# Kernel tuning notes

Measured on AMD Instinct MI355X. Metric: run time of the kernel, lower is better.

## Reference

```python
import jax, jax.numpy as jnp
import numpy as np

N1 = 50000
N2 = 50000
NN = 16
NI = 64
ND = 128


def setup_inputs() -> dict:
    key = jax.random.key(0)
    ks = jax.random.split(key, 12)
    inp = {
        "features1": jax.random.normal(ks[0], (N1, NI), dtype=jnp.float32),
        "features2": jax.random.normal(ks[1], (N2, NI), dtype=jnp.float32),
        "x1": jax.random.normal(ks[2], (N1, 3), dtype=jnp.float32),
        "x2": jax.random.normal(ks[3], (N2, 3), dtype=jnp.float32),
        "nuv1": jax.random.normal(ks[4], (N1, 3, 3), dtype=jnp.float32),
        "nuv2": jax.random.normal(ks[5], (N2, 3, 3), dtype=jnp.float32),
        "topk": jax.random.randint(ks[6], (N1, NN), 0, N2, dtype=jnp.int64),
        # query_f params: Linear(2*Ni, Nd) -> ELU -> Linear(Nd, Nd) -> ELU
        "W1": jax.random.normal(ks[7], (2 * NI, ND), dtype=jnp.float32) * (1.0 / np.sqrt(2 * NI)),
        "b1": jnp.zeros((ND,), dtype=jnp.float32),
        "W2": jax.random.normal(ks[8], (ND, ND), dtype=jnp.float32) * (1.0 / np.sqrt(ND)),
        "b2": jnp.zeros((ND,), dtype=jnp.float32),
        "radius": jnp.float32(1.0),
    }
    return inp


def reference(features1, features2, x1, x2, nuv1, nuv2, topk, W1, b1, W2, b2, radius):
    # gather neighbor features: [N1, nn, Ni]
    feats_nn = features2[topk]
    # concat with self features broadcast over neighbor axis: [N1, nn, 2*Ni]
    feat_self = jnp.broadcast_to(features1[:, None, :], feats_nn.shape)
    h = jnp.concatenate([feats_nn, feat_self], axis=-1)
    # small fused MLP (query_f)
    h = jax.nn.elu(h @ W1 + b1)
    h = jax.nn.elu(h @ W2 + b2)  # [N1, nn, Nd]
    # distance-weighted aggregation
    x_nn = x2[topk]                          # [N1, nn, 3]
    orient = x_nn - x1[:, None, :]
    dis2 = jnp.sum(orient * orient, axis=2)  # [N1, nn]
    w = jnp.exp(-dis2 / (2.0 * radius * radius))
    w = jnp.where(topk == 0, jnp.float32(0.0), w)  # mask padded (index-0) neighbors
    # weighted matmul reduction: [N1, Nd]
    out = jnp.einsum("nk,nkd->nd", w, h)
    return out
```

## Files before the change

kernel.cpp:

```cpp
#include <hip/hip_runtime.h>

#define N1C 50000
#define N2C 50000
#define NNC 16
#define NIC 64
#define NDC 128
#define QB  8
#define MR  128
#define FELEMS (N1C * NIC)

typedef __bf16 bf16x8 __attribute__((ext_vector_type(8)));
typedef float f32x4 __attribute__((ext_vector_type(4)));
typedef unsigned u32x4 __attribute__((ext_vector_type(4)));

#if defined(__has_builtin)
#if __has_builtin(__builtin_amdgcn_cvt_pk_bf16_f32)
#define HAVE_PK_BF16 1
#endif
#endif

#ifdef HAVE_PK_BF16
typedef __bf16 bf16x2 __attribute__((ext_vector_type(2)));
static __device__ __forceinline__ unsigned int pkbf(float a, float b) {
    bf16x2 r = __builtin_amdgcn_cvt_pk_bf16_f32(a, b);
    return __builtin_bit_cast(unsigned int, r);
}
#else
static __device__ __forceinline__ unsigned short f2bf_sw(float f) {
    unsigned int u = __builtin_bit_cast(unsigned int, f);
    u += 0x7fffu + ((u >> 16) & 1u);
    return (unsigned short)(u >> 16);
}
static __device__ __forceinline__ unsigned int pkbf(float a, float b) {
    return (unsigned int)f2bf_sw(a) | ((unsigned int)f2bf_sw(b) << 16);
}
#endif

static __device__ __forceinline__ float elu(float x) {
    return x > 0.f ? x : __expf(x) - 1.f;
}

__global__ void prep_w(const float* __restrict__ W1, const float* __restrict__ W2,
                       unsigned short* __restrict__ wsW) {
    const int idx = blockIdx.x * 256 + threadIdx.x;
    const int m   = idx >> 14;
    const int o   = idx & 16383;
    const int d   = o >> 7;
    const int k   = o & 127;
    const float* W = m ? W2 : W1;
    wsW[idx] = (unsigned short)pkbf(W[(size_t)k * NDC + d], 0.f);
}

__global__ void prep_f(const float* __restrict__ f1, const float* __restrict__ f2,
                       unsigned short* __restrict__ dst) {
    const int g = blockIdx.x * 256 + threadIdx.x;
    const size_t base = (size_t)g * 8;
    const float* src = (base < FELEMS) ? (f1 + base) : (f2 + base - FELEMS);
    const float4 v0 = *(const float4*)src;
    const float4 v1 = *(const float4*)(src + 4);
    uint4 o;
    o.x = pkbf(v0.x, v0.y);
    o.y = pkbf(v0.z, v0.w);
    o.z = pkbf(v1.x, v1.y);
    o.w = pkbf(v1.z, v1.w);
    *(uint4*)(dst + base) = o;
}

static __device__ __forceinline__ int swz(int o) {
    return (o & ~15) | ((o + (o >> 4)) & 15);
}

__global__ __launch_bounds__(256, 4)
void fused_knn_mlp(const unsigned short* __restrict__ f1b,
                   const unsigned short* __restrict__ f2b,
                   const float* __restrict__ x1,
                   const float* __restrict__ x2,
                   const int*   __restrict__ topk,
                   const float* __restrict__ b1,
                   const float* __restrict__ b2,
                   const float* __restrict__ radius,
                   const unsigned short* __restrict__ wsW,
                   float* __restrict__ out)
{
    __shared__ uint4 sW[2048];

    const int tid  = threadIdx.x;
    const int blk  = blockIdx.x;
    const int lane = tid & 63;
    const int wave = tid >> 6;
    const int quad = lane >> 4;
    const int l16  = lane & 15;
    const int rloc = wave * 32 + l16;

    const int idx0 = topk[blk * MR + rloc];
    const int idx1 = topk[blk * MR + rloc + 16];
    const int q0   = blk * QB + wave * 2;
    const int q1   = q0 + 1;

    uint4 xf0[4], xf1[4];
    #pragma unroll
    for (int ks = 0; ks < 2; ++ks) {
        xf0[ks] = *(const uint4*)(f2b + (size_t)idx0 * NIC + ks * 32 + quad * 8);
        xf1[ks] = *(const uint4*)(f2b + (size_t)idx1 * NIC + ks * 32 + quad * 8);
        xf0[ks + 2] = *(const uint4*)(f1b + (size_t)q0 * NIC + ks * 32 + quad * 8);
        xf1[ks + 2] = *(const uint4*)(f1b + (size_t)q1 * NIC + ks * 32 + quad * 8);
    }

    {
        const uint4* wp = (const uint4*)wsW;
        #pragma unroll
        for (int it = 0; it < 8; ++it) {
            const int o = it * 256 + tid;
            sW[swz(o)] = wp[o];
        }
    }

    float wg0, wg1;
    {
        const float rr = radius[0];
        const float inv2r2 = 1.f / (2.f * rr * rr);
        const float dx0 = x2[idx0 * 3 + 0] - x1[q0 * 3 + 0];
        const float dy0 = x2[idx0 * 3 + 1] - x1[q0 * 3 + 1];
        const float dz0 = x2[idx0 * 3 + 2] - x1[q0 * 3 + 2];
        const float dx1 = x2[idx1 * 3 + 0] - x1[q1 * 3 + 0];
        const float dy1 = x2[idx1 * 3 + 1] - x1[q1 * 3 + 1];
        const float dz1 = x2[idx1 * 3 + 2] - x1[q1 * 3 + 2];
        wg0 = (idx0 == 0) ? 0.f : __expf(-(dx0 * dx0 + dy0 * dy0 + dz0 * dz0) * inv2r2);
        wg1 = (idx1 == 0) ? 0.f : __expf(-(dx1 * dx1 + dy1 * dy1 + dz1 * dz1) * inv2r2);
    }

    __syncthreads();

    f32x4 acc[8][2];
    #pragma unroll
    for (int mt = 0; mt < 8; ++mt) {
        acc[mt][0] = (f32x4){0.f, 0.f, 0.f, 0.f};
        acc[mt][1] = acc[mt][0];
    }
    #pragma unroll
    for (int ks = 0; ks < 4; ++ks) {
        const bf16x8 x0 = __builtin_bit_cast(bf16x8, xf0[ks]);
        const bf16x8 x1v = __builtin_bit_cast(bf16x8, xf1[ks]);
        #pragma unroll
        for (int mt = 0; mt < 8; ++mt) {
            const bf16x8 a = *(const bf16x8*)&sW[(mt * 16 + l16) * 16 + ((ks * 4 + quad + l16) & 15)];
            acc[mt][0] = __builtin_amdgcn_mfma_f32_16x16x32_bf16(a, x0, acc[mt][0], 0, 0, 0);
            acc[mt][1] = __builtin_amdgcn_mfma_f32_16x16x32_bf16(a, x1v, acc[mt][1], 0, 0, 0);
        }
    }

    __syncthreads();

    uint4 w2t[8];
    {
        const uint4* wp2 = ((const uint4*)wsW) + 2048;
        #pragma unroll
        for (int it = 0; it < 8; ++it)
            w2t[it] = wp2[it * 256 + tid];
    }

    unsigned P[8][2][2];
    #pragma unroll
    for (int mt = 0; mt < 8; ++mt) {
        const float4 b1v = *(const float4*)(b1 + mt * 16 + quad * 4);
        #pragma unroll
        for (int nt = 0; nt < 2; ++nt) {
            P[mt][nt][0] = pkbf(elu(acc[mt][nt][0] + b1v.x), elu(acc[mt][nt][1] + b1v.y));
            P[mt][nt][1] = pkbf(elu(acc[mt][nt][2] + b1v.z), elu(acc[mt][nt][3] + b1v.w));
        }
    }

    #pragma unroll
    for (int it = 0; it < 8; ++it)
        sW[swz(it * 256 + tid)] = w2t[it];
    __syncthreads();

    f32x4 acc2[2][8];
    #pragma unroll
    for (int nt2 = 0; nt2 < 8; ++nt2) {
        acc2[0][nt2] = (f32x4){0.f, 0.f, 0.f, 0.f};
        acc2[1][nt2] = acc2[0][nt2];
    }
    #pragma unroll
    for (int ks = 0; ks < 4; ++ks) {
        u32x4 a2[2];
        #pragma unroll
        for (int mt2 = 0; mt2 < 2; ++mt2) {
            #pragma unroll
            for (int u = 0; u < 4; ++u) {
                const int src = (((quad * 2) + (u >> 1)) & 3) * 16 + l16;
                const unsigned lo = __shfl(P[2 * ks][mt2][u & 1], src, 64);
                const unsigned hi = __shfl(P[2 * ks + 1][mt2][u & 1], src, 64);
                a2[mt2][u] = (quad & 2) ? hi : lo;
            }
        }
        const bf16x8 af0 = __builtin_bit_cast(bf16x8, a2[0]);
        const bf16x8 af1 = __builtin_bit_cast(bf16x8, a2[1]);
        #pragma unroll
        for (int nt2 = 0; nt2 < 8; ++nt2) {
            const bf16x8 b = *(const bf16x8*)&sW[(nt2 * 16 + l16) * 16 + ((ks * 4 + quad + l16) & 15)];
            acc2[0][nt2] = __builtin_amdgcn_mfma_f32_16x16x32_bf16(af0, b, acc2[0][nt2], 0, 0, 0);
            acc2[1][nt2] = __builtin_amdgcn_mfma_f32_16x16x32_bf16(af1, b, acc2[1][nt2], 0, 0, 0);
        }
    }

    float wk0[4], wk1[4];
    #pragma unroll
    for (int reg = 0; reg < 4; ++reg) {
        const int src = (lane & 48) | (quad * 4 + reg);
        wk0[reg] = __shfl(wg0, src, 64);
        wk1[reg] = __shfl(wg1, src, 64);
    }
    #pragma unroll
    for (int mt2 = 0; mt2 < 2; ++mt2) {
        #pragma unroll
        for (int nt2 = 0; nt2 < 8; ++nt2) {
            const int d2 = nt2 * 16 + l16;
            const float bb = b2[d2];
            float s;
            if (mt2 == 0)
                s = elu(acc2[0][nt2][0] + bb) * wk0[0] + elu(acc2[0][nt2][1] + bb) * wk0[1]
                  + elu(acc2[0][nt2][2] + bb) * wk0[2] + elu(acc2[0][nt2][3] + bb) * wk0[3];
            else
                s = elu(acc2[1][nt2][0] + bb) * wk1[0] + elu(acc2[1][nt2][1] + bb) * wk1[1]
                  + elu(acc2[1][nt2][2] + bb) * wk1[2] + elu(acc2[1][nt2][3] + bb) * wk1[3];
            s += __shfl_xor(s, 16, 64);
            s += __shfl_xor(s, 32, 64);
            if (lane < 16) {
                out[(size_t)(blk * QB + wave * 2 + mt2) * NDC + d2] = s;
            }
        }
    }
}

extern "C" void kernel_launch(void* const* d_in, const int* in_sizes, int n_in,
                              void* d_out, int out_size, void* d_ws, size_t ws_size,
                              hipStream_t stream) {
    const float* features1 = (const float*)d_in[0];
    const float* features2 = (const float*)d_in[1];
    const float* x1        = (const float*)d_in[2];
    const float* x2        = (const float*)d_in[3];
    const int*   topk      = (const int*)d_in[6];
    const float* W1        = (const float*)d_in[7];
    const float* b1        = (const float*)d_in[8];
    const float* W2        = (const float*)d_in[9];
    const float* b2        = (const float*)d_in[10];
    const float* radius    = (const float*)d_in[11];
    float* out = (float*)d_out;

    unsigned short* wsW = (unsigned short*)d_ws;
    unsigned short* f1b = wsW + 32768;
    unsigned short* f2b = f1b + FELEMS;

    prep_w<<<dim3(128), 256, 0, stream>>>(W1, W2, wsW);
    prep_f<<<dim3(3125), 256, 0, stream>>>(features1, features2, f1b);
    fused_knn_mlp<<<dim3(N1C / QB), 256, 0, stream>>>(f1b, f2b, x1, x2, topk,
                                                      b1, b2, radius, wsW, out);
}
```

Measured before the change: 223.5 us.

## Stage weights via direct global-to-LDS loads in MFMA fragment order

Weights are pre-permuted on the host-side prep kernel into per-lane MFMA fragment order, so each LDS read becomes a contiguous lane-indexed 16-byte access without swizzling. Weight tiles are staged with global_load_lds (direct global-to-LDS) instead of passing through registers, and the W2 register prefetch is dropped. The first GEMM is restructured to compute two M-tiles at a time and apply bias+ELU immediately, cutting live accumulator registers. This trades the earlier overlap of W2 loading with the ELU epilogue for lower register pressure and fewer VGPR round trips.

```diff
diff --git a/kernel.cpp b/kernel.cpp
--- a/kernel.cpp
+++ b/kernel.cpp
@@ -40,13 +40,28 @@
     return x > 0.f ? x : __expf(x) - 1.f;
 }
 
+static __device__ __forceinline__ void stage16(const uint4* gsrc_lane, uint4* ldst_base) {
+#if defined(__has_builtin) && __has_builtin(__builtin_amdgcn_global_load_lds)
+    __builtin_amdgcn_global_load_lds(
+        (const __attribute__((address_space(1))) void*)gsrc_lane,
+        (__attribute__((address_space(3))) void*)ldst_base, 16, 0, 0);
+#else
+    ldst_base[threadIdx.x & 63] = *gsrc_lane;
+#endif
+}
+
 __global__ void prep_w(const float* __restrict__ W1, const float* __restrict__ W2,
                        unsigned short* __restrict__ wsW) {
-    const int idx = blockIdx.x * 256 + threadIdx.x;
-    const int m   = idx >> 14;
-    const int o   = idx & 16383;
-    const int d   = o >> 7;
-    const int k   = o & 127;
+    const int idx  = blockIdx.x * 256 + threadIdx.x;
+    const int m    = idx >> 14;
+    const int o    = idx & 16383;
+    const int j    = o & 7;
+    const int lane = (o >> 3) & 63;
+    const int ksmt = o >> 9;
+    const int ks   = ksmt & 3;
+    const int mt   = ksmt >> 2;
+    const int d = mt * 16 + (lane & 15);
+    const int k = ks * 32 + (lane >> 4) * 8 + j;
     const float* W = m ? W2 : W1;
     wsW[idx] = (unsigned short)pkbf(W[(size_t)k * NDC + d], 0.f);
 }
@@ -66,10 +81,6 @@
     *(uint4*)(dst + base) = o;
 }
 
-static __device__ __forceinline__ int swz(int o) {
-    return (o & ~15) | ((o + (o >> 4)) & 15);
-}
-
 __global__ __launch_bounds__(256, 4)
 void fused_knn_mlp(const unsigned short* __restrict__ f1b,
                    const unsigned short* __restrict__ f2b,
@@ -92,6 +103,15 @@
     const int l16  = lane & 15;
     const int rloc = wave * 32 + l16;
 
+    const uint4* wp1 = (const uint4*)wsW;
+    const uint4* wp2 = wp1 + 2048;
+
+    #pragma unroll
+    for (int it = 0; it < 8; ++it) {
+        const int base = wave * 512 + it * 64;
+        stage16(wp1 + base + lane, sW + base);
+    }
+
     const int idx0 = topk[blk * MR + rloc];
     const int idx1 = topk[blk * MR + rloc + 16];
     const int q0   = blk * QB + wave * 2;
@@ -104,15 +124,6 @@
         xf1[ks] = *(const uint4*)(f2b + (size_t)idx1 * NIC + ks * 32 + quad * 8);
         xf0[ks + 2] = *(const uint4*)(f1b + (size_t)q0 * NIC + ks * 32 + quad * 8);
         xf1[ks + 2] = *(const uint4*)(f1b + (size_t)q1 * NIC + ks * 32 + quad * 8);
-    }
-
-    {
-        const uint4* wp = (const uint4*)wsW;
-        #pragma unroll
-        for (int it = 0; it < 8; ++it) {
-            const int o = it * 256 + tid;
-            sW[swz(o)] = wp[o];
-        }
     }
 
     float wg0, wg1;
@@ -131,48 +142,46 @@
 
     __syncthreads();
 
-    f32x4 acc[8][2];
-    #pragma unroll
-    for (int mt = 0; mt < 8; ++mt) {
-        acc[mt][0] = (f32x4){0.f, 0.f, 0.f, 0.f};
-        acc[mt][1] = acc[mt][0];
-    }
-    #pragma unroll
-    for (int ks = 0; ks < 4; ++ks) {
-        const bf16x8 x0 = __builtin_bit_cast(bf16x8, xf0[ks]);
-        const bf16x8 x1v = __builtin_bit_cast(bf16x8, xf1[ks]);
-        #pragma unroll
-        for (int mt = 0; mt < 8; ++mt) {
-            const bf16x8 a = *(const bf16x8*)&sW[(mt * 16 + l16) * 16 + ((ks * 4 + quad + l16) & 15)];
-            acc[mt][0] = __builtin_amdgcn_mfma_f32_16x16x32_bf16(a, x0, acc[mt][0], 0, 0, 0);
-            acc[mt][1] = __builtin_amdgcn_mfma_f32_16x16x32_bf16(a, x1v, acc[mt][1], 0, 0, 0);
+    unsigned P[8][2][2];
+    #pragma unroll
+    for (int mp = 0; mp < 4; ++mp) {
+        f32x4 accp[2][2];
+        #pragma unroll
+        for (int mi = 0; mi < 2; ++mi) {
+            accp[mi][0] = (f32x4){0.f, 0.f, 0.f, 0.f};
+            accp[mi][1] = accp[mi][0];
+        }
+        #pragma unroll
+        for (int ks = 0; ks < 4; ++ks) {
+            const bf16x8 x0  = __builtin_bit_cast(bf16x8, xf0[ks]);
+            const bf16x8 x1v = __builtin_bit_cast(bf16x8, xf1[ks]);
+            #pragma unroll
+            for (int mi = 0; mi < 2; ++mi) {
+                const int mt = mp * 2 + mi;
+                const bf16x8 a = *(const bf16x8*)&sW[(mt * 4 + ks) * 64 + lane];
+                accp[mi][0] = __builtin_amdgcn_mfma_f32_16x16x32_bf16(a, x0,  accp[mi][0], 0, 0, 0);
+                accp[mi][1] = __builtin_amdgcn_mfma_f32_16x16x32_bf16(a, x1v, accp[mi][1], 0, 0, 0);
+            }
+        }
+        #pragma unroll
+        for (int mi = 0; mi < 2; ++mi) {
+            const int mt = mp * 2 + mi;
+            const float4 b1v = *(const float4*)(b1 + mt * 16 + quad * 4);
+            #pragma unroll
+            for (int nt = 0; nt < 2; ++nt) {
+                P[mt][nt][0] = pkbf(elu(accp[mi][nt][0] + b1v.x), elu(accp[mi][nt][1] + b1v.y));
+                P[mt][nt][1] = pkbf(elu(accp[mi][nt][2] + b1v.z), elu(accp[mi][nt][3] + b1v.w));
+            }
         }
     }
 
     __syncthreads();
 
-    uint4 w2t[8];
-    {
-        const uint4* wp2 = ((const uint4*)wsW) + 2048;
-        #pragma unroll
-        for (int it = 0; it < 8; ++it)
-            w2t[it] = wp2[it * 256 + tid];
-    }
-
-    unsigned P[8][2][2];
-    #pragma unroll
-    for (int mt = 0; mt < 8; ++mt) {
-        const float4 b1v = *(const float4*)(b1 + mt * 16 + quad * 4);
-        #pragma unroll
-        for (int nt = 0; nt < 2; ++nt) {
-            P[mt][nt][0] = pkbf(elu(acc[mt][nt][0] + b1v.x), elu(acc[mt][nt][1] + b1v.y));
-            P[mt][nt][1] = pkbf(elu(acc[mt][nt][2] + b1v.z), elu(acc[mt][nt][3] + b1v.w));
-        }
-    }
-
-    #pragma unroll
-    for (int it = 0; it < 8; ++it)
-        sW[swz(it * 256 + tid)] = w2t[it];
+    #pragma unroll
+    for (int it = 0; it < 8; ++it) {
+        const int base = wave * 512 + it * 64;
+        stage16(wp2 + base + lane, sW + base);
+    }
     __syncthreads();
 
     f32x4 acc2[2][8];
@@ -198,7 +207,7 @@
         const bf16x8 af1 = __builtin_bit_cast(bf16x8, a2[1]);
         #pragma unroll
         for (int nt2 = 0; nt2 < 8; ++nt2) {
-            const bf16x8 b = *(const bf16x8*)&sW[(nt2 * 16 + l16) * 16 + ((ks * 4 + quad + l16) & 15)];
+            const bf16x8 b = *(const bf16x8*)&sW[(nt2 * 4 + ks) * 64 + lane];
             acc2[0][nt2] = __builtin_amdgcn_mfma_f32_16x16x32_bf16(af0, b, acc2[0][nt2], 0, 0, 0);
             acc2[1][nt2] = __builtin_amdgcn_mfma_f32_16x16x32_bf16(af1, b, acc2[1][nt2], 0, 0, 0);
         }
```

After: 198.3 us. 1.13x faster.
